# Optimization experiments

Measured on AMD Instinct MI355X. Metric: run time of the kernel, lower is better.

The kernel has to match this reference:

```python
import jax, jax.numpy as jnp
import numpy as np

D_MODEL = 512
NUM_HEADS = 8
D_HEAD = 64
BATCH = 2
SEQ = 2048
NEG_BIG = 1.0e10


def setup_inputs() -> dict:
    key = jax.random.key(0)
    k1, k2, k3, k4, k5 = jax.random.split(key, 5)
    scale = D_MODEL ** -0.5
    return {
        "x": jax.random.normal(k1, (BATCH, SEQ, D_MODEL), dtype=jnp.float32),
        "W_Q": jax.random.normal(k2, (NUM_HEADS, D_HEAD, D_MODEL), dtype=jnp.float32) * scale,
        "W_K": jax.random.normal(k3, (NUM_HEADS, D_HEAD, D_MODEL), dtype=jnp.float32) * scale,
        "W_V": jax.random.normal(k4, (NUM_HEADS, D_HEAD, D_MODEL), dtype=jnp.float32) * scale,
        "W_O": jax.random.normal(k5, (D_MODEL, D_HEAD * NUM_HEADS), dtype=jnp.float32) * scale,
    }


def reference(x, W_Q, W_K, W_V, W_O):
    b, n, d = x.shape
    # q,k,v: [b, heads, pos, d_head]
    q = jnp.einsum('ihd,bpd->biph', W_Q, x)
    k = jnp.einsum('ihd,bpd->biph', W_K, x)
    v = jnp.einsum('ihd,bpd->biph', W_V, x)
    # scores: [b, heads, q_pos, k_pos]
    scores = jnp.einsum('biph,biqh->biqp', k, q)
    tril = jnp.tril(jnp.ones((n, n), dtype=scores.dtype))   # keep p <= q
    triu = jnp.triu(jnp.ones((n, n), dtype=scores.dtype))   # buffer 'mask'
    # Faithful to source: tril(scores) - 1e10 * (1 - triu)
    masked = scores * tril - NEG_BIG * (1.0 - triu)
    attn = jax.nn.softmax(masked / (D_HEAD ** 0.5), axis=-1)
    z = jnp.einsum('biph,biqp->biqh', v, attn)               # [b, i, q, h]
    z_flat = jnp.transpose(z, (0, 2, 1, 3)).reshape(b, n, -1)  # [b, q, i*h]
    out = jnp.einsum('df,bqf->bqd', W_O, z_flat)
    return out
```

## Files before the change

kernel.cpp:

```cpp
#include <hip/hip_runtime.h>
#include <stdint.h>

#define BATCH 2
#define SEQ 2048
#define DM 512
#define NH 8
#define DH 64
#define MROWS (BATCH * SEQ)
#define NCHUNK 64
#define CHUNK (SEQ / NCHUNK)

typedef __attribute__((ext_vector_type(8))) short bf16x8;
typedef __attribute__((ext_vector_type(4))) float f32x4;

__device__ __forceinline__ unsigned short f2bf(float f) {
    union { float f; uint32_t u; } x; x.f = f;
    uint32_t r = x.u + 0x7fffu + ((x.u >> 16) & 1u);
    return (unsigned short)(r >> 16);
}
__device__ __forceinline__ float bf2f(unsigned short s) {
    union { uint32_t u; float f; } x; x.u = ((uint32_t)s) << 16;
    return x.f;
}

__device__ __forceinline__ void gl_lds16(const void* g, void* l) {
    __builtin_amdgcn_global_load_lds(
        (const __attribute__((address_space(1))) void*)(uintptr_t)g,
        (__attribute__((address_space(3))) void*)(uint32_t)(uintptr_t)l,
        16, 0, 0);
}

__global__ void cvt_all(const float4* __restrict__ x,
                        const float4* __restrict__ Wq, const float4* __restrict__ Wk,
                        const float4* __restrict__ Wv, const float4* __restrict__ Wo,
                        ushort4* __restrict__ xb, ushort4* __restrict__ wb) {
    int i = blockIdx.x * blockDim.x + threadIdx.x;
    float4 v; ushort4* dst; int off;
    if (i < 524288) {
        v = x[i]; dst = xb; off = i;
    } else {
        int j = i - 524288;
        if (j < 131072) {
            int head = j >> 14, rp = (j >> 7) & 127, colq = j & 127;
            v = (rp < 64) ? Wq[head * 8192 + rp * 128 + colq]
                          : Wk[head * 8192 + (rp - 64) * 128 + colq];
        } else if (j < 196608) {
            v = Wv[j - 131072];
        } else {
            v = Wo[j - 196608];
        }
        dst = wb; off = j;
    }
    ushort4 o; o.x = f2bf(v.x); o.y = f2bf(v.y); o.z = f2bf(v.z); o.w = f2bf(v.w);
    dst[off] = o;
}

__global__ __launch_bounds__(256) void proj(
    const unsigned short* __restrict__ xb, const unsigned short* __restrict__ wb,
    float* __restrict__ cA, float* __restrict__ cW,
    unsigned short* __restrict__ V, float* __restrict__ csum)
{
    __shared__ __align__(16) unsigned short S[256 * 32];
    const int t = threadIdx.x, lane = t & 63, wave = t >> 6;
    const int lr = lane >> 2, lc = (lane & 3) * 8;
    const int bid = blockIdx.x;
    const int wm = wave * 32;
    const int kcol = (lane >> 4) * 8;
    const int l15 = lane & 15;

    if (bid < 256) {
        const int head = bid & 7, m0 = (bid >> 3) * 128;
        const unsigned short* B = wb + head * 65536;
        const unsigned short* gb[4];
#pragma unroll
        for (int r = 0; r < 4; r++) {
            int grow = r * 64 + wave * 16 + lr;
            gb[r] = (grow < 128) ? xb + (size_t)(m0 + grow) * 512 + lc
                                 : B + (size_t)(grow - 128) * 512 + lc;
        }
        f32x4 acc[2][8];
#pragma unroll
        for (int i = 0; i < 2; i++)
#pragma unroll
            for (int j = 0; j < 8; j++) { f32x4 z = {0.f,0.f,0.f,0.f}; acc[i][j] = z; }
        for (int k0 = 0; k0 < 512; k0 += 32) {
            __syncthreads();
#pragma unroll
            for (int r = 0; r < 4; r++)
                gl_lds16(gb[r] + k0, S + (r * 64 + wave * 16) * 32);
            __syncthreads();
            bf16x8 af[2], bfr[8];
#pragma unroll
            for (int i = 0; i < 2; i++)
                af[i] = *(const bf16x8*)(S + (wm + i * 16 + l15) * 32 + kcol);
#pragma unroll
            for (int j = 0; j < 8; j++)
                bfr[j] = *(const bf16x8*)(S + (128 + j * 16 + l15) * 32 + kcol);
#pragma unroll
            for (int i = 0; i < 2; i++)
#pragma unroll
                for (int j = 0; j < 8; j++)
                    acc[i][j] = __builtin_amdgcn_mfma_f32_16x16x32_bf16(af[i], bfr[j], acc[i][j], 0, 0, 0);
        }
#pragma unroll
        for (int i = 0; i < 2; i++)
#pragma unroll
            for (int r = 0; r < 4; r++) {
                float d = 0.f;
#pragma unroll
                for (int j = 0; j < 4; j++) d += acc[i][j][r] * acc[i][j + 4][r];
                d += __shfl_xor(d, 1); d += __shfl_xor(d, 2);
                d += __shfl_xor(d, 4); d += __shfl_xor(d, 8);
                if (l15 == 0) {
                    int row = m0 + wm + i * 16 + (lane >> 4) * 4 + r;
                    int p = row & (SEQ - 1);
                    float dd = d * 0.125f;
                    float M = fmaxf(dd, 0.f);
                    float a = expf(dd - M), e0 = expf(-M);
                    float Z = a + (float)(SEQ - 1 - p) * e0;
                    cA[row * NH + head] = a / Z;
                    cW[row * NH + head] = e0 / Z;
                }
            }
    } else {
        const int b2 = bid - 256;
        const int head = b2 & 7, m0 = (b2 >> 3) * 128, n0 = head * 64;
        const unsigned short* B = wb + 524288 + (size_t)n0 * 512;
        const unsigned short* gb[3];
#pragma unroll
        for (int r = 0; r < 3; r++) {
            int grow = r * 64 + wave * 16 + lr;
            gb[r] = (grow < 128) ? xb + (size_t)(m0 + grow) * 512 + lc
                                 : B + (size_t)(grow - 128) * 512 + lc;
        }
        f32x4 acc[2][4];
#pragma unroll
        for (int i = 0; i < 2; i++)
#pragma unroll
            for (int j = 0; j < 4; j++) { f32x4 z = {0.f,0.f,0.f,0.f}; acc[i][j] = z; }
        for (int k0 = 0; k0 < 512; k0 += 32) {
            __syncthreads();
#pragma unroll
            for (int r = 0; r < 3; r++)
                gl_lds16(gb[r] + k0, S + (r * 64 + wave * 16) * 32);
            __syncthreads();
            bf16x8 af[2], bfr[4];
#pragma unroll
            for (int i = 0; i < 2; i++)
                af[i] = *(const bf16x8*)(S + (wm + i * 16 + l15) * 32 + kcol);
#pragma unroll
            for (int j = 0; j < 4; j++)
                bfr[j] = *(const bf16x8*)(S + (128 + j * 16 + l15) * 32 + kcol);
#pragma unroll
            for (int i = 0; i < 2; i++)
#pragma unroll
                for (int j = 0; j < 4; j++)
                    acc[i][j] = __builtin_amdgcn_mfma_f32_16x16x32_bf16(af[i], bfr[j], acc[i][j], 0, 0, 0);
        }
        const int crow = m0 + wm + (lane >> 4) * 4;
#pragma unroll
        for (int i = 0; i < 2; i++)
#pragma unroll
            for (int j = 0; j < 4; j++)
#pragma unroll
                for (int r = 0; r < 4; r++)
                    V[(size_t)(crow + i * 16 + r) * DM + n0 + j * 16 + l15] = f2bf(acc[i][j][r]);
        float s[4];
#pragma unroll
        for (int j = 0; j < 4; j++) {
            s[j] = 0.f;
#pragma unroll
            for (int i = 0; i < 2; i++)
#pragma unroll
                for (int r = 0; r < 4; r++) s[j] += acc[i][j][r];
            s[j] += __shfl_xor(s[j], 16);
            s[j] += __shfl_xor(s[j], 32);
        }
        if (lane < 16) {
            int bi = (m0 >> 11) * NH + head;
            int chunk = ((m0 & (SEQ - 1)) >> 5) + wave;
#pragma unroll
            for (int j = 0; j < 4; j++)
                csum[(bi * NCHUNK + chunk) * 64 + j * 16 + lane] = s[j];
        }
    }
}

__global__ __launch_bounds__(256) void zbuild(
    const unsigned short* __restrict__ V, const float* __restrict__ csum,
    const float* __restrict__ cA, const float* __restrict__ cW,
    unsigned short* __restrict__ Zb) {
    int ci = blockIdx.x * 4 + (threadIdx.x >> 6);
    int h = threadIdx.x & 63;
    int c = ci & (NCHUNK - 1), bi = ci >> 6;
    int i = bi & 7, b = bi >> 3;
    float r = 0.f;
    for (int cc = c + 1; cc < NCHUNK; cc++) r += csum[((bi << 6) + cc) * 64 + h];
    for (int j = CHUNK - 1; j >= 0; j--) {
        int p = c * CHUNK + j;
        size_t row = (size_t)(b * SEQ + p);
        float v = bf2f(V[row * DM + i * DH + h]);
        float a = cA[row * NH + i], w = cW[row * NH + i];
        Zb[row * DM + i * DH + h] = f2bf(fmaf(a, v, w * r));
        r += v;
    }
}

template<int TM, int TN, int WM, int WN>
__global__ __launch_bounds__(256) void gemm_bt(
    const unsigned short* __restrict__ A, const unsigned short* __restrict__ B,
    float* __restrict__ C, int M, int N, int K)
{
    constexpr int ROWS = TM + TN;
    constexpr int ROUNDS = ROWS / 64;
    constexpr int MI = WM / 16, NJ = WN / 16;
    constexpr int WAVES_N = TN / WN;
    __shared__ __align__(16) unsigned short S[ROWS * 32];
    const int t = threadIdx.x, lane = t & 63, wave = t >> 6;
    const int wm = (wave / WAVES_N) * WM, wn = (wave % WAVES_N) * WN;
    const int m0 = blockIdx.x * TM, n0 = blockIdx.y * TN;
    const int lr = lane >> 2, lc = (lane & 3) * 8;

    const unsigned short* gbase[ROUNDS];
#pragma unroll
    for (int r = 0; r < ROUNDS; r++) {
        int grow = r * 64 + wave * 16 + lr;
        gbase[r] = (grow < TM) ? A + (size_t)(m0 + grow) * K + lc
                               : B + (size_t)(n0 + grow - TM) * K + lc;
    }

    f32x4 acc[MI][NJ];
#pragma unroll
    for (int i = 0; i < MI; i++)
#pragma unroll
        for (int j = 0; j < NJ; j++) { f32x4 z = {0.f,0.f,0.f,0.f}; acc[i][j] = z; }

    const int mrow = wm + (lane & 15);
    const int nrow = TM + wn + (lane & 15);
    const int kcol = (lane >> 4) * 8;

    for (int k0 = 0; k0 < K; k0 += 32) {
        __syncthreads();
#pragma unroll
        for (int r = 0; r < ROUNDS; r++)
            gl_lds16(gbase[r] + k0, S + (r * 64 + wave * 16) * 32);
        __syncthreads();
        bf16x8 af[MI], bfr[NJ];
#pragma unroll
        for (int i = 0; i < MI; i++)
            af[i] = *(const bf16x8*)(S + (mrow + i * 16) * 32 + kcol);
#pragma unroll
        for (int j = 0; j < NJ; j++)
            bfr[j] = *(const bf16x8*)(S + (nrow + j * 16) * 32 + kcol);
#pragma unroll
        for (int i = 0; i < MI; i++)
#pragma unroll
            for (int j = 0; j < NJ; j++)
                acc[i][j] = __builtin_amdgcn_mfma_f32_16x16x32_bf16(af[i], bfr[j], acc[i][j], 0, 0, 0);
    }
    const int crow = m0 + wm + (lane >> 4) * 4;
    const int ccol = n0 + wn + (lane & 15);
#pragma unroll
    for (int i = 0; i < MI; i++)
#pragma unroll
        for (int j = 0; j < NJ; j++)
#pragma unroll
            for (int r = 0; r < 4; r++)
                C[(size_t)(crow + i * 16 + r) * N + ccol + j * 16] = acc[i][j][r];
}

extern "C" void kernel_launch(void* const* d_in, const int* in_sizes, int n_in,
                              void* d_out, int out_size, void* d_ws, size_t ws_size,
                              hipStream_t stream) {
    const float* x  = (const float*)d_in[0];
    const float* Wq = (const float*)d_in[1];
    const float* Wk = (const float*)d_in[2];
    const float* Wv = (const float*)d_in[3];
    const float* Wo = (const float*)d_in[4];
    float* out = (float*)d_out;
    char* ws = (char*)d_ws;

    unsigned short* xb = (unsigned short*)(ws);
    unsigned short* wb = (unsigned short*)(ws + 4194304);
    unsigned short* V  = (unsigned short*)(ws + 6291456);
    float* cA = (float*)(ws + 10485760);
    float* cW = (float*)(ws + 10616832);
    float* cs = (float*)(ws + 10747904);
    unsigned short* Zb = (unsigned short*)(ws + 11010048);

    cvt_all<<<3072, 256, 0, stream>>>((const float4*)x, (const float4*)Wq,
                                      (const float4*)Wk, (const float4*)Wv,
                                      (const float4*)Wo, (ushort4*)xb, (ushort4*)wb);
    proj<<<512, 256, 0, stream>>>(xb, wb, cA, cW, V, cs);
    zbuild<<<256, 256, 0, stream>>>(V, cs, cA, cW, Zb);
    gemm_bt<64, 64, 32, 32><<<dim3(64, 8, 1), 256, 0, stream>>>(
        Zb, wb + 786432, out, MROWS, DM, DM);
}
```

Baseline: 115.6 us.

## Double-buffer LDS tiles with XOR swizzle and BK=64 in projection and GEMM kernels

Replaces the single-buffered BK=32 LDS loop in the proj and gemm_bt kernels with a double-buffered BK=64 pipeline. The next tile's global-to-LDS loads are issued before computing on the current tile, and one barrier per iteration replaces two. LDS rows are XOR-swizzled in 16-byte chunks to avoid bank conflicts on the fragment reads. This doubles LDS usage per block, which may lower occupancy, and relies on a manual vmcnt wait plus s_barrier for correctness.

After: 103.6 us. -10.3%, faster.

```diff
diff --git a/kernel.cpp b/kernel.cpp
--- a/kernel.cpp
+++ b/kernel.cpp
@@ -60,48 +60,71 @@
     float* __restrict__ cA, float* __restrict__ cW,
     unsigned short* __restrict__ V, float* __restrict__ csum)
 {
-    __shared__ __align__(16) unsigned short S[256 * 32];
+    __shared__ __align__(16) unsigned short S[2 * 256 * 64];
     const int t = threadIdx.x, lane = t & 63, wave = t >> 6;
-    const int lr = lane >> 2, lc = (lane & 3) * 8;
+    const int lr = lane >> 3;
+    const int csrc = ((lane & 7) ^ lr) * 8;
+    const int l15 = lane & 15, q = lane >> 4;
     const int bid = blockIdx.x;
     const int wm = wave * 32;
-    const int kcol = (lane >> 4) * 8;
-    const int l15 = lane & 15;
 
     if (bid < 256) {
+        constexpr int TE = 256 * 64;
         const int head = bid & 7, m0 = (bid >> 3) * 128;
-        const unsigned short* B = wb + head * 65536;
-        const unsigned short* gb[4];
-#pragma unroll
-        for (int r = 0; r < 4; r++) {
-            int grow = r * 64 + wave * 16 + lr;
-            gb[r] = (grow < 128) ? xb + (size_t)(m0 + grow) * 512 + lc
-                                 : B + (size_t)(grow - 128) * 512 + lc;
+        const unsigned short* Bw = wb + head * 65536;
+        const unsigned short* gb[8];
+#pragma unroll
+        for (int r = 0; r < 8; r++) {
+            int s = r * 4 + wave, g = s * 8 + lr;
+            gb[r] = (g < 128) ? xb + (size_t)(m0 + g) * 512 + csrc
+                              : Bw + (size_t)(g - 128) * 512 + csrc;
         }
         f32x4 acc[2][8];
 #pragma unroll
         for (int i = 0; i < 2; i++)
 #pragma unroll
             for (int j = 0; j < 8; j++) { f32x4 z = {0.f,0.f,0.f,0.f}; acc[i][j] = z; }
-        for (int k0 = 0; k0 < 512; k0 += 32) {
-            __syncthreads();
-#pragma unroll
-            for (int r = 0; r < 4; r++)
-                gl_lds16(gb[r] + k0, S + (r * 64 + wave * 16) * 32);
-            __syncthreads();
-            bf16x8 af[2], bfr[8];
-#pragma unroll
-            for (int i = 0; i < 2; i++)
-                af[i] = *(const bf16x8*)(S + (wm + i * 16 + l15) * 32 + kcol);
-#pragma unroll
-            for (int j = 0; j < 8; j++)
-                bfr[j] = *(const bf16x8*)(S + (128 + j * 16 + l15) * 32 + kcol);
-#pragma unroll
-            for (int i = 0; i < 2; i++)
-#pragma unroll
-                for (int j = 0; j < 8; j++)
-                    acc[i][j] = __builtin_amdgcn_mfma_f32_16x16x32_bf16(af[i], bfr[j], acc[i][j], 0, 0, 0);
-        }
+
+        auto stage = [&](unsigned short* Sb, int k0) {
+#pragma unroll
+            for (int r = 0; r < 8; r++)
+                gl_lds16(gb[r] + k0, Sb + (r * 4 + wave) * 512);
+        };
+        auto compute = [&](const unsigned short* Sb) {
+#pragma unroll
+            for (int h = 0; h < 2; h++) {
+                bf16x8 af[2], bfr[8];
+#pragma unroll
+                for (int i = 0; i < 2; i++) {
+                    int R = wm + i * 16 + l15;
+                    af[i] = *(const bf16x8*)(Sb + R * 64 + (((q + 4 * h) ^ (R & 7)) * 8));
+                }
+#pragma unroll
+                for (int j = 0; j < 8; j++) {
+                    int R = 128 + j * 16 + l15;
+                    bfr[j] = *(const bf16x8*)(Sb + R * 64 + (((q + 4 * h) ^ (R & 7)) * 8));
+                }
+#pragma unroll
+                for (int i = 0; i < 2; i++)
+#pragma unroll
+                    for (int j = 0; j < 8; j++)
+                        acc[i][j] = __builtin_amdgcn_mfma_f32_16x16x32_bf16(af[i], bfr[j], acc[i][j], 0, 0, 0);
+            }
+        };
+
+        stage(S, 0);
+        asm volatile("s_waitcnt vmcnt(0)" ::: "memory");
+        __builtin_amdgcn_s_barrier();
+        int cur = 0;
+        for (int k0 = 64; k0 < 512; k0 += 64) {
+            stage(S + (cur ^ 1) * TE, k0);
+            compute(S + cur * TE);
+            asm volatile("s_waitcnt vmcnt(0)" ::: "memory");
+            __builtin_amdgcn_s_barrier();
+            cur ^= 1;
+        }
+        compute(S + cur * TE);
+
 #pragma unroll
         for (int i = 0; i < 2; i++)
 #pragma unroll
@@ -123,40 +146,63 @@
                 }
             }
     } else {
+        constexpr int TE = 192 * 64;
         const int b2 = bid - 256;
         const int head = b2 & 7, m0 = (b2 >> 3) * 128, n0 = head * 64;
-        const unsigned short* B = wb + 524288 + (size_t)n0 * 512;
-        const unsigned short* gb[3];
-#pragma unroll
-        for (int r = 0; r < 3; r++) {
-            int grow = r * 64 + wave * 16 + lr;
-            gb[r] = (grow < 128) ? xb + (size_t)(m0 + grow) * 512 + lc
-                                 : B + (size_t)(grow - 128) * 512 + lc;
+        const unsigned short* Bv = wb + 524288 + (size_t)n0 * 512;
+        const unsigned short* gb[6];
+#pragma unroll
+        for (int r = 0; r < 6; r++) {
+            int s = r * 4 + wave, g = s * 8 + lr;
+            gb[r] = (g < 128) ? xb + (size_t)(m0 + g) * 512 + csrc
+                              : Bv + (size_t)(g - 128) * 512 + csrc;
         }
         f32x4 acc[2][4];
 #pragma unroll
         for (int i = 0; i < 2; i++)
 #pragma unroll
             for (int j = 0; j < 4; j++) { f32x4 z = {0.f,0.f,0.f,0.f}; acc[i][j] = z; }
-        for (int k0 = 0; k0 < 512; k0 += 32) {
-            __syncthreads();
-#pragma unroll
-            for (int r = 0; r < 3; r++)
-                gl_lds16(gb[r] + k0, S + (r * 64 + wave * 16) * 32);
-            __syncthreads();
-            bf16x8 af[2], bfr[4];
-#pragma unroll
-            for (int i = 0; i < 2; i++)
-                af[i] = *(const bf16x8*)(S + (wm + i * 16 + l15) * 32 + kcol);
-#pragma unroll
-            for (int j = 0; j < 4; j++)
-                bfr[j] = *(const bf16x8*)(S + (128 + j * 16 + l15) * 32 + kcol);
-#pragma unroll
-            for (int i = 0; i < 2; i++)
-#pragma unroll
-                for (int j = 0; j < 4; j++)
-                    acc[i][j] = __builtin_amdgcn_mfma_f32_16x16x32_bf16(af[i], bfr[j], acc[i][j], 0, 0, 0);
-        }
+
+        auto stage = [&](unsigned short* Sb, int k0) {
+#pragma unroll
+            for (int r = 0; r < 6; r++)
+                gl_lds16(gb[r] + k0, Sb + (r * 4 + wave) * 512);
+        };
+        auto compute = [&](const unsigned short* Sb) {
+#pragma unroll
+            for (int h = 0; h < 2; h++) {
+                bf16x8 af[2], bfr[4];
+#pragma unroll
+                for (int i = 0; i < 2; i++) {
+                    int R = wm + i * 16 + l15;
+                    af[i] = *(const bf16x8*)(Sb + R * 64 + (((q + 4 * h) ^ (R & 7)) * 8));
+                }
+#pragma unroll
+                for (int j = 0; j < 4; j++) {
+                    int R = 128 + j * 16 + l15;
+                    bfr[j] = *(const bf16x8*)(Sb + R * 64 + (((q + 4 * h) ^ (R & 7)) * 8));
+                }
+#pragma unroll
+                for (int i = 0; i < 2; i++)
+#pragma unroll
+                    for (int j = 0; j < 4; j++)
+                        acc[i][j] = __builtin_amdgcn_mfma_f32_16x16x32_bf16(af[i], bfr[j], acc[i][j], 0, 0, 0);
+            }
+        };
+
+        stage(S, 0);
+        asm volatile("s_waitcnt vmcnt(0)" ::: "memory");
+        __builtin_amdgcn_s_barrier();
+        int cur = 0;
+        for (int k0 = 64; k0 < 512; k0 += 64) {
+            stage(S + (cur ^ 1) * TE, k0);
+            compute(S + cur * TE);
+            asm volatile("s_waitcnt vmcnt(0)" ::: "memory");
+            __builtin_amdgcn_s_barrier();
+            cur ^= 1;
+        }
+        compute(S + cur * TE);
+
         const int crow = m0 + wm + (lane >> 4) * 4;
 #pragma unroll
         for (int i = 0; i < 2; i++)
@@ -212,21 +258,24 @@
     float* __restrict__ C, int M, int N, int K)
 {
     constexpr int ROWS = TM + TN;
-    constexpr int ROUNDS = ROWS / 64;
+    constexpr int SPW = ROWS / 32;
     constexpr int MI = WM / 16, NJ = WN / 16;
     constexpr int WAVES_N = TN / WN;
-    __shared__ __align__(16) unsigned short S[ROWS * 32];
+    constexpr int TE = ROWS * 64;
+    __shared__ __align__(16) unsigned short S[2 * TE];
     const int t = threadIdx.x, lane = t & 63, wave = t >> 6;
     const int wm = (wave / WAVES_N) * WM, wn = (wave % WAVES_N) * WN;
     const int m0 = blockIdx.x * TM, n0 = blockIdx.y * TN;
-    const int lr = lane >> 2, lc = (lane & 3) * 8;
-
-    const unsigned short* gbase[ROUNDS];
-#pragma unroll
-    for (int r = 0; r < ROUNDS; r++) {
-        int grow = r * 64 + wave * 16 + lr;
-        gbase[r] = (grow < TM) ? A + (size_t)(m0 + grow) * K + lc
-                               : B + (size_t)(n0 + grow - TM) * K + lc;
+    const int lr = lane >> 3;
+    const int csrc = ((lane & 7) ^ lr) * 8;
+    const int l15 = lane & 15, q = lane >> 4;
+
+    const unsigned short* gb[SPW];
+#pragma unroll
+    for (int r = 0; r < SPW; r++) {
+        int s = r * 4 + wave, g = s * 8 + lr;
+        gb[r] = (g < TM) ? A + (size_t)(m0 + g) * K + csrc
+                         : B + (size_t)(n0 + g - TM) * K + csrc;
     }
 
     f32x4 acc[MI][NJ];
@@ -235,29 +284,46 @@
 #pragma unroll
         for (int j = 0; j < NJ; j++) { f32x4 z = {0.f,0.f,0.f,0.f}; acc[i][j] = z; }
 
-    const int mrow = wm + (lane & 15);
-    const int nrow = TM + wn + (lane & 15);
-    const int kcol = (lane >> 4) * 8;
-
-    for (int k0 = 0; k0 < K; k0 += 32) {
-        __syncthreads();
-#pragma unroll
-        for (int r = 0; r < ROUNDS; r++)
-            gl_lds16(gbase[r] + k0, S + (r * 64 + wave * 16) * 32);
-        __syncthreads();
-        bf16x8 af[MI], bfr[NJ];
-#pragma unroll
-        for (int i = 0; i < MI; i++)
-            af[i] = *(const bf16x8*)(S + (mrow + i * 16) * 32 + kcol);
-#pragma unroll
-        for (int j = 0; j < NJ; j++)
-            bfr[j] = *(const bf16x8*)(S + (nrow + j * 16) * 32 + kcol);
-#pragma unroll
-        for (int i = 0; i < MI; i++)
-#pragma unroll
-            for (int j = 0; j < NJ; j++)
-                acc[i][j] = __builtin_amdgcn_mfma_f32_16x16x32_bf16(af[i], bfr[j], acc[i][j], 0, 0, 0);
-    }
+    auto stage = [&](unsigned short* Sb, int k0) {
+#pragma unroll
+        for (int r = 0; r < SPW; r++)
+            gl_lds16(gb[r] + k0, Sb + (r * 4 + wave) * 512);
+    };
+    auto compute = [&](const unsigned short* Sb) {
+#pragma unroll
+        for (int h = 0; h < 2; h++) {
+            bf16x8 af[MI], bfr[NJ];
+#pragma unroll
+            for (int i = 0; i < MI; i++) {
+                int R = wm + i * 16 + l15;
+                af[i] = *(const bf16x8*)(Sb + R * 64 + (((q + 4 * h) ^ (R & 7)) * 8));
+            }
+#pragma unroll
+            for (int j = 0; j < NJ; j++) {
+                int R = TM + wn + j * 16 + l15;
+                bfr[j] = *(const bf16x8*)(Sb + R * 64 + (((q + 4 * h) ^ (R & 7)) * 8));
+            }
+#pragma unroll
+            for (int i = 0; i < MI; i++)
+#pragma unroll
+                for (int j = 0; j < NJ; j++)
+                    acc[i][j] = __builtin_amdgcn_mfma_f32_16x16x32_bf16(af[i], bfr[j], acc[i][j], 0, 0, 0);
+        }
+    };
+
+    stage(S, 0);
+    asm volatile("s_waitcnt vmcnt(0)" ::: "memory");
+    __builtin_amdgcn_s_barrier();
+    int cur = 0;
+    for (int k0 = 64; k0 < K; k0 += 64) {
+        stage(S + (cur ^ 1) * TE, k0);
+        compute(S + cur * TE);
+        asm volatile("s_waitcnt vmcnt(0)" ::: "memory");
+        __builtin_amdgcn_s_barrier();
+        cur ^= 1;
+    }
+    compute(S + cur * TE);
+
     const int crow = m0 + wm + (lane >> 4) * 4;
     const int ccol = n0 + wn + (lane & 15);
 #pragma unroll
```
